# Optimization experiments

Measured on AMD Instinct MI355X. Metric: run time of the kernel, lower is better.

## Reference

```python
import jax, jax.numpy as jnp
import numpy as np

INPUT, HIDDEN = 128, 64
B, T = 512, 1024


def _lstm_dir(x, Wih, Whh, b):
    """Single-direction LSTM (PyTorch gate order i,f,g,o). x: [B,T,I] -> [B,T,H]."""
    Bn = x.shape[0]
    H = Whh.shape[1]
    # precompute input contributions for all timesteps: [B,T,4H]
    xg = jnp.einsum('bti,gi->btg', x, Wih) + b

    def step(carry, g_t):
        h, c = carry
        g = g_t + h @ Whh.T  # [B,4H]
        i, f, gg, o = jnp.split(g, 4, axis=-1)
        c = jax.nn.sigmoid(f) * c + jax.nn.sigmoid(i) * jnp.tanh(gg)
        h = jax.nn.sigmoid(o) * jnp.tanh(c)
        return (h, c), h

    h0 = jnp.zeros((Bn, H), x.dtype)
    (_, _), hs = jax.lax.scan(step, (h0, h0), jnp.swapaxes(xg, 0, 1))
    return jnp.swapaxes(hs, 0, 1)  # [B,T,H]


def setup_inputs() -> dict:
    key = jax.random.key(0)
    ks = jax.random.split(key, 9)
    s_ih = 1.0 / np.sqrt(HIDDEN)
    def u(k, shape):
        return jax.random.uniform(k, shape, jnp.float32, -s_ih, s_ih)
    return {
        'x': jax.random.normal(ks[0], (B, T, INPUT), jnp.float32),
        'Wih_f': u(ks[1], (4 * HIDDEN, INPUT)),
        'Whh_f': u(ks[2], (4 * HIDDEN, HIDDEN)),
        'b_f': u(ks[3], (4 * HIDDEN,)),   # b_ih + b_hh folded (same math)
        'Wih_b': u(ks[4], (4 * HIDDEN, INPUT)),
        'Whh_b': u(ks[5], (4 * HIDDEN, HIDDEN)),
        'b_b': u(ks[6], (4 * HIDDEN,)),
    }


def reference(x, Wih_f, Whh_f, b_f, Wih_b, Whh_b, b_b):
    # forward returns the full bidirectional sequence output [B,T,2H]
    out_f = _lstm_dir(x, Wih_f, Whh_f, b_f)
    out_b = _lstm_dir(x[:, ::-1], Wih_b, Whh_b, b_b)[:, ::-1]
    return jnp.concatenate([out_f, out_b], axis=-1)
```

## Files before the change

### kernel.cpp

```cpp
#include <hip/hip_runtime.h>

#define T_LEN 1024
#define IN_DIM 128
#define HID 64
#define CH 8
#define NCH (T_LEN / CH)
#define XSTR 160
#define HSTR 96
#define OSTR 72

typedef __attribute__((ext_vector_type(8))) short short8;
typedef __attribute__((ext_vector_type(4))) float floatx4;
typedef __attribute__((ext_vector_type(2))) unsigned uintx2;

__device__ __forceinline__ unsigned short f2bf(float v) {
    union { float f; unsigned u; } a; a.f = v;
    unsigned r = a.u + 0x7FFFu + ((a.u >> 16) & 1u);
    return (unsigned short)(r >> 16);
}

__device__ __forceinline__ short8 cvt8(const float* p) {
    short8 r;
#pragma unroll
    for (int j = 0; j < 8; ++j) r[j] = (short)f2bf(p[j]);
    return r;
}

__device__ __forceinline__ float i2f(int v) { union { int i; float f; } u; u.i = v; return u.f; }
__device__ __forceinline__ int   f2i(float v) { union { float f; int i; } u; u.f = v; return u.i; }

#define LOG2E 1.44269504088896f
__device__ __forceinline__ float sigm(float x) {
    return __builtin_amdgcn_rcpf(1.0f + __builtin_amdgcn_exp2f(x * -LOG2E));
}
__device__ __forceinline__ float tanh_(float x) {
    return 2.0f * __builtin_amdgcn_rcpf(1.0f + __builtin_amdgcn_exp2f(x * -2.0f * LOG2E)) - 1.0f;
}

__global__ __launch_bounds__(256, 1) void lstm_bidir(
    const float* __restrict__ x,
    const float* __restrict__ WihF, const float* __restrict__ WhhF, const float* __restrict__ bF,
    const float* __restrict__ WihB, const float* __restrict__ WhhB, const float* __restrict__ bB,
    float* __restrict__ out)
{
    const int tid  = threadIdx.x;
    const int w    = tid >> 6;
    const int lane = tid & 63;
    const int nloc = lane & 15;
    const int quad = lane >> 4;
    const int bid  = blockIdx.x;
    const int dir  = bid & 1;
    const int b0   = (bid >> 1) * 4;

    const float* Wih  = dir ? WihB : WihF;
    const float* Whh  = dir ? WhhB : WhhF;
    const float* bias = dir ? bB   : bF;

    __shared__ __align__(16) unsigned short xch[2][CH][4 * XSTR];
    __shared__ __align__(16) unsigned short h_s[2][4 * HSTR];
    __shared__ __align__(16) float obuf[2][CH][4][OSTR];

    for (int i = tid; i < 2 * 4 * HSTR; i += 256) ((unsigned short*)h_s)[i] = 0;

    short8 wihf[4][4];
    short8 whhf[4][2];
    float  bv[4];
#pragma unroll
    for (int gc = 0; gc < 4; ++gc) {
        const int row = gc * 64 + w * 16 + nloc;
        bv[gc] = bias[row];
#pragma unroll
        for (int kf = 0; kf < 4; ++kf)
            wihf[gc][kf] = cvt8(Wih + row * IN_DIM + kf * 32 + quad * 8);
#pragma unroll
        for (int kf = 0; kf < 2; ++kf)
            whhf[gc][kf] = cvt8(Whh + row * HID + kf * 32 + quad * 8);
    }

    auto tmap = [&](int s) {
        int ss = s < T_LEN - 1 ? s : T_LEN - 1;
        return dir ? (T_LEN - 1 - ss) : ss;
    };

    const int g   = tid >> 5;
    const int l32 = tid & 31;

#pragma unroll
    for (int i = 0; i < 4; ++i) {
        floatx4 v = *(const floatx4*)(x + (size_t)(b0 + i) * T_LEN * IN_DIM
                                        + (size_t)tmap(g) * IN_DIM + l32 * 4);
        unsigned lo = (unsigned)f2bf(v.x) | ((unsigned)f2bf(v.y) << 16);
        unsigned hi = (unsigned)f2bf(v.z) | ((unsigned)f2bf(v.w) << 16);
        uintx2 p = {lo, hi};
        *(uintx2*)&xch[0][g][i * XSTR + l32 * 4] = p;
    }

    float c = 0.f;
    const bool q1 = (quad & 1) != 0;
    const bool q2 = (quad & 2) != 0;

    __syncthreads();

    floatx4 TBA[4], TBB[4];
#pragma unroll
    for (int gc = 0; gc < 4; ++gc) TBA[gc] = (floatx4){bv[gc], bv[gc], bv[gc], bv[gc]};
#pragma unroll
    for (int kf = 0; kf < 4; ++kf) {
        short8 xa = *(const short8*)&xch[0][nloc >> 2][(nloc & 3) * XSTR + kf * 32 + quad * 8];
#pragma unroll
        for (int gc = 0; gc < 4; ++gc)
            TBA[gc] = __builtin_amdgcn_mfma_f32_16x16x32_bf16(xa, wihf[gc][kf], TBA[gc], 0, 0, 0);
    }

    floatx4 stg[4];

    auto flushPrev = [&](int chkPrev) {
        const int pb  = chkPrev & 1;
        const int fs  = tid >> 5;
        const int fr  = (tid & 31) >> 3;
        const int fu  = (tid & 7) * 8;
        const float* src = &obuf[pb][fs][fr][fu];
        floatx4 v0 = *(const floatx4*)(src);
        floatx4 v1 = *(const floatx4*)(src + 4);
        const int tg = tmap(chkPrev * CH + fs);
        float* dst = out + ((size_t)(b0 + fr) * T_LEN + tg) * 128 + dir * HID + fu;
        *(floatx4*)(dst)     = v0;
        *(floatx4*)(dst + 4) = v1;
    };

    auto stepT = [&](int sl, int chk, int cbuf, floatx4* TBuse, floatx4* TBbuild) {
        const int cur  = sl & 1;
        const int tloc = sl & 3;

        if (sl == 0) {
            if (chk > 0) flushPrev(chk - 1);
            if (chk + 1 < NCH) {
                const int tn = (chk + 1) * CH + g;
#pragma unroll
                for (int i = 0; i < 4; ++i)
                    stg[i] = *(const floatx4*)(x + (size_t)(b0 + i) * T_LEN * IN_DIM
                                                 + (size_t)tmap(tn) * IN_DIM + l32 * 4);
            }
        }
        if (sl == 1 && chk + 1 < NCH) {
#pragma unroll
            for (int i = 0; i < 4; ++i) {
                unsigned lo = (unsigned)f2bf(stg[i].x) | ((unsigned)f2bf(stg[i].y) << 16);
                unsigned hi = (unsigned)f2bf(stg[i].z) | ((unsigned)f2bf(stg[i].w) << 16);
                uintx2 p = {lo, hi};
                *(uintx2*)&xch[cbuf ^ 1][g][i * XSTR + l32 * 4] = p;
            }
        }

        float xg[4];
        {
            const int addr = (tloc * 16 + nloc) * 4;
#pragma unroll
            for (int gc = 0; gc < 4; ++gc) {
                float f0 = i2f(__builtin_amdgcn_ds_bpermute(addr, f2i(TBuse[gc][0])));
                float f1 = i2f(__builtin_amdgcn_ds_bpermute(addr, f2i(TBuse[gc][1])));
                float f2 = i2f(__builtin_amdgcn_ds_bpermute(addr, f2i(TBuse[gc][2])));
                float f3 = i2f(__builtin_amdgcn_ds_bpermute(addr, f2i(TBuse[gc][3])));
                float a  = q1 ? f1 : f0;
                float b_ = q1 ? f3 : f2;
                xg[gc] = q2 ? b_ : a;
            }
        }

        short8 ha[2];
        const unsigned short* hb = &h_s[cur][(nloc >> 2) * HSTR + quad * 8];
#pragma unroll
        for (int kf = 0; kf < 2; ++kf) ha[kf] = *(const short8*)(hb + kf * 32);

        floatx4 acc[4];
#pragma unroll
        for (int gc = 0; gc < 4; ++gc) acc[gc] = (floatx4){xg[gc], xg[gc], xg[gc], xg[gc]};
#pragma unroll
        for (int gc = 0; gc < 4; ++gc)
            acc[gc] = __builtin_amdgcn_mfma_f32_16x16x32_bf16(ha[0], whhf[gc][0], acc[gc], 0, 0, 0);
#pragma unroll
        for (int gc = 0; gc < 4; ++gc)
            acc[gc] = __builtin_amdgcn_mfma_f32_16x16x32_bf16(ha[1], whhf[gc][1], acc[gc], 0, 0, 0);

        {
            const unsigned short* xb = (sl < 4)
                ? &xch[cbuf][4 + (nloc >> 2)][(nloc & 3) * XSTR + tloc * 32 + quad * 8]
                : &xch[cbuf ^ 1][nloc >> 2][(nloc & 3) * XSTR + tloc * 32 + quad * 8];
            short8 xa = *(const short8*)xb;
            if (tloc == 0) {
#pragma unroll
                for (int gc = 0; gc < 4; ++gc)
                    TBbuild[gc] = (floatx4){bv[gc], bv[gc], bv[gc], bv[gc]};
            }
#pragma unroll
            for (int gc = 0; gc < 4; ++gc)
                TBbuild[gc] = __builtin_amdgcn_mfma_f32_16x16x32_bf16(xa, wihf[gc][tloc], TBbuild[gc], 0, 0, 0);
        }

        {
            float iv = sigm(acc[0][0]);
            float fv = sigm(acc[1][0]);
            float gv = tanh_(acc[2][0]);
            float ov = sigm(acc[3][0]);
            c = fv * c + iv * gv;
            float hv = ov * tanh_(c);
            obuf[cbuf][sl][quad][w * 16 + nloc] = hv;
            h_s[cur ^ 1][quad * HSTR + w * 16 + nloc] = f2bf(hv);
        }
        __syncthreads();
    };

    for (int chk = 0; chk < NCH; ++chk) {
        const int cbuf = chk & 1;
#pragma unroll
        for (int sl = 0; sl < CH; ++sl) {
            if (sl < 4) stepT(sl, chk, cbuf, TBA, TBB);
            else        stepT(sl, chk, cbuf, TBB, TBA);
        }
    }
    flushPrev(NCH - 1);
}

extern "C" void kernel_launch(void* const* d_in, const int* in_sizes, int n_in,
                              void* d_out, int out_size, void* d_ws, size_t ws_size,
                              hipStream_t stream) {
    const float* x    = (const float*)d_in[0];
    const float* WihF = (const float*)d_in[1];
    const float* WhhF = (const float*)d_in[2];
    const float* bF   = (const float*)d_in[3];
    const float* WihB = (const float*)d_in[4];
    const float* WhhB = (const float*)d_in[5];
    const float* bB   = (const float*)d_in[6];
    float* out = (float*)d_out;

    lstm_bidir<<<dim3(256), dim3(256), 0, stream>>>(x, WihF, WhhF, bF, WihB, WhhB, bB, out);
}
```

Before: 872.8 us.

## Repack staged x into XOR-swizzled LDS layout so MFMA output needs no bpermute

Changes the shared-memory layout of the staged input chunk so that each MFMA row is (batch, timestep-in-quarter) ordered, letting each lane pick its precomputed input-gate value directly from its accumulator register (TBuse[gc][tloc]) instead of doing 16 ds_bpermute shuffles plus selects per step. The x staging now loads 16 contiguous floats per thread and writes two swizzled short8 vectors to avoid bank conflicts. It also skips the input-projection MFMA build for the nonexistent chunk after the last one. The risk is a subtle mapping error in the swizzle or row assignment that breaks correctness.

Result: faster. 753.2 us (-13.7%).

```diff
diff --git a/kernel.cpp b/kernel.cpp
--- a/kernel.cpp
+++ b/kernel.cpp
@@ -5,13 +5,13 @@
 #define HID 64
 #define CH 8
 #define NCH (T_LEN / CH)
-#define XSTR 160
 #define HSTR 96
 #define OSTR 72
+#define PKROW 128
+#define PKSZ  (16 * PKROW)
 
 typedef __attribute__((ext_vector_type(8))) short short8;
 typedef __attribute__((ext_vector_type(4))) float floatx4;
-typedef __attribute__((ext_vector_type(2))) unsigned uintx2;
 
 __device__ __forceinline__ unsigned short f2bf(float v) {
     union { float f; unsigned u; } a; a.f = v;
@@ -25,9 +25,6 @@
     for (int j = 0; j < 8; ++j) r[j] = (short)f2bf(p[j]);
     return r;
 }
-
-__device__ __forceinline__ float i2f(int v) { union { int i; float f; } u; u.i = v; return u.f; }
-__device__ __forceinline__ int   f2i(float v) { union { float f; int i; } u; u.f = v; return u.i; }
 
 #define LOG2E 1.44269504088896f
 __device__ __forceinline__ float sigm(float x) {
@@ -56,7 +53,7 @@
     const float* Whh  = dir ? WhhB : WhhF;
     const float* bias = dir ? bB   : bF;
 
-    __shared__ __align__(16) unsigned short xch[2][CH][4 * XSTR];
+    __shared__ __align__(16) unsigned short xpk[2][2][PKSZ];
     __shared__ __align__(16) unsigned short h_s[2][4 * HSTR];
     __shared__ __align__(16) float obuf[2][CH][4][OSTR];
 
@@ -84,20 +81,26 @@
 
     const int g   = tid >> 5;
     const int l32 = tid & 31;
-
-#pragma unroll
-    for (int i = 0; i < 4; ++i) {
-        floatx4 v = *(const floatx4*)(x + (size_t)(b0 + i) * T_LEN * IN_DIM
-                                        + (size_t)tmap(g) * IN_DIM + l32 * 4);
-        unsigned lo = (unsigned)f2bf(v.x) | ((unsigned)f2bf(v.y) << 16);
-        unsigned hi = (unsigned)f2bf(v.z) | ((unsigned)f2bf(v.w) << 16);
-        uintx2 p = {lo, hi};
-        *(uintx2*)&xch[0][g][i * XSTR + l32 * 4] = p;
+    const int sb  = l32 >> 3;
+    const int sp  = l32 & 7;
+    const int srow = sb * 4 + (g & 3);
+    const int spk  = g >> 2;
+    const int wo0 = srow * PKROW + (((2 * sp)     ^ (srow & 7)) * 8);
+    const int wo1 = srow * PKROW + (((2 * sp + 1) ^ (srow & 7)) * 8);
+    const float* xsrc = x + (size_t)(b0 + sb) * T_LEN * IN_DIM + sp * 16;
+
+    int ro[4];
+#pragma unroll
+    for (int kf = 0; kf < 4; ++kf)
+        ro[kf] = nloc * PKROW + ((((kf * 4 + quad) ^ (nloc & 7))) * 8);
+
+    {
+        const float* p = xsrc + (size_t)tmap(g) * IN_DIM;
+        *(short8*)&xpk[0][spk][wo0] = cvt8(p);
+        *(short8*)&xpk[0][spk][wo1] = cvt8(p + 8);
     }
 
     float c = 0.f;
-    const bool q1 = (quad & 1) != 0;
-    const bool q2 = (quad & 2) != 0;
 
     __syncthreads();
 
@@ -106,7 +109,7 @@
     for (int gc = 0; gc < 4; ++gc) TBA[gc] = (floatx4){bv[gc], bv[gc], bv[gc], bv[gc]};
 #pragma unroll
     for (int kf = 0; kf < 4; ++kf) {
-        short8 xa = *(const short8*)&xch[0][nloc >> 2][(nloc & 3) * XSTR + kf * 32 + quad * 8];
+        short8 xa = *(const short8*)(&xpk[0][0][0] + ro[kf]);
 #pragma unroll
         for (int gc = 0; gc < 4; ++gc)
             TBA[gc] = __builtin_amdgcn_mfma_f32_16x16x32_bf16(xa, wihf[gc][kf], TBA[gc], 0, 0, 0);
@@ -135,36 +138,15 @@
         if (sl == 0) {
             if (chk > 0) flushPrev(chk - 1);
             if (chk + 1 < NCH) {
-                const int tn = (chk + 1) * CH + g;
+                const float* p = xsrc + (size_t)tmap((chk + 1) * CH + g) * IN_DIM;
 #pragma unroll
                 for (int i = 0; i < 4; ++i)
-                    stg[i] = *(const floatx4*)(x + (size_t)(b0 + i) * T_LEN * IN_DIM
-                                                 + (size_t)tmap(tn) * IN_DIM + l32 * 4);
+                    stg[i] = *(const floatx4*)(p + i * 4);
             }
         }
         if (sl == 1 && chk + 1 < NCH) {
-#pragma unroll
-            for (int i = 0; i < 4; ++i) {
-                unsigned lo = (unsigned)f2bf(stg[i].x) | ((unsigned)f2bf(stg[i].y) << 16);
-                unsigned hi = (unsigned)f2bf(stg[i].z) | ((unsigned)f2bf(stg[i].w) << 16);
-                uintx2 p = {lo, hi};
-                *(uintx2*)&xch[cbuf ^ 1][g][i * XSTR + l32 * 4] = p;
-            }
-        }
-
-        float xg[4];
-        {
-            const int addr = (tloc * 16 + nloc) * 4;
-#pragma unroll
-            for (int gc = 0; gc < 4; ++gc) {
-                float f0 = i2f(__builtin_amdgcn_ds_bpermute(addr, f2i(TBuse[gc][0])));
-                float f1 = i2f(__builtin_amdgcn_ds_bpermute(addr, f2i(TBuse[gc][1])));
-                float f2 = i2f(__builtin_amdgcn_ds_bpermute(addr, f2i(TBuse[gc][2])));
-                float f3 = i2f(__builtin_amdgcn_ds_bpermute(addr, f2i(TBuse[gc][3])));
-                float a  = q1 ? f1 : f0;
-                float b_ = q1 ? f3 : f2;
-                xg[gc] = q2 ? b_ : a;
-            }
+            *(short8*)&xpk[cbuf ^ 1][spk][wo0] = cvt8((const float*)&stg[0]);
+            *(short8*)&xpk[cbuf ^ 1][spk][wo1] = cvt8((const float*)&stg[2]);
         }
 
         short8 ha[2];
@@ -172,9 +154,16 @@
 #pragma unroll
         for (int kf = 0; kf < 2; ++kf) ha[kf] = *(const short8*)(hb + kf * 32);
 
+        const bool doBuild = (sl < 4) || (chk + 1 < NCH);
+        const unsigned short* pkb = (sl < 4) ? &xpk[cbuf][1][0] : &xpk[cbuf ^ 1][0][0];
+        short8 xa = *(const short8*)(pkb + ro[tloc]);
+
         floatx4 acc[4];
 #pragma unroll
-        for (int gc = 0; gc < 4; ++gc) acc[gc] = (floatx4){xg[gc], xg[gc], xg[gc], xg[gc]};
+        for (int gc = 0; gc < 4; ++gc) {
+            const float xg = TBuse[gc][tloc];
+            acc[gc] = (floatx4){xg, xg, xg, xg};
+        }
 #pragma unroll
         for (int gc = 0; gc < 4; ++gc)
             acc[gc] = __builtin_amdgcn_mfma_f32_16x16x32_bf16(ha[0], whhf[gc][0], acc[gc], 0, 0, 0);
@@ -182,11 +171,7 @@
         for (int gc = 0; gc < 4; ++gc)
             acc[gc] = __builtin_amdgcn_mfma_f32_16x16x32_bf16(ha[1], whhf[gc][1], acc[gc], 0, 0, 0);
 
-        {
-            const unsigned short* xb = (sl < 4)
-                ? &xch[cbuf][4 + (nloc >> 2)][(nloc & 3) * XSTR + tloc * 32 + quad * 8]
-                : &xch[cbuf ^ 1][nloc >> 2][(nloc & 3) * XSTR + tloc * 32 + quad * 8];
-            short8 xa = *(const short8*)xb;
+        if (doBuild) {
             if (tloc == 0) {
 #pragma unroll
                 for (int gc = 0; gc < 4; ++gc)
```
